# Kernel optimization log

Measured on AMD Instinct MI355X. Metric: run time of the kernel, lower is better.

Reference implementation:

```python
import jax, jax.numpy as jnp
import numpy as np

M = 5
N = 3
NUM_EPOC = 500
LR = 0.01


def setup_inputs() -> dict:
    key = jax.random.key(0)
    k1, k2, k3, k4, k5 = jax.random.split(key, 5)
    x = jax.random.normal(k1, (8, 32, 32, 128), dtype=jnp.float32)
    weight = jax.random.normal(k2, (3, 3, 128, 256), dtype=jnp.float32) * 0.05
    shiftPara = jax.random.normal(k3, (N,), dtype=jnp.float32) * 0.1
    beta = jax.random.normal(k4, (N,), dtype=jnp.float32)
    alphas_init = jax.random.normal(k5, (M,), dtype=jnp.float32)
    return {"x": x, "weight": weight, "shiftPara": shiftPara, "beta": beta, "alphas_init": alphas_init}


def _binary_weights(w):
    # w: (kh, kw, Cin, Cout). sign(W - mean + shift_i * std), shift_i in linspace(-1, 1, M)
    mean = jnp.mean(w)
    var = jnp.var(w)
    shifts = (-1.0 + jnp.arange(M, dtype=jnp.float32) * (2.0 / (M - 1))) * jnp.sqrt(var)  # (M,)
    return jnp.sign((w - mean)[None] + shifts.reshape(M, 1, 1, 1, 1))  # (M, kh, kw, Cin, Cout)


def _alphas(w, bw, alphas_init):
    # 500-step OLS gradient descent, faithful to the original loop
    flat_w = w.reshape(-1)            # (K,)
    flat_b = bw.reshape(M, -1)        # (M, K)
    K = flat_w.shape[0]

    def step(a, _):
        resid = flat_b.T @ a - flat_w            # (K,)
        grad = (flat_b @ resid) / K              # (M,)
        return a - LR * grad, None

    a, _ = jax.lax.scan(step, alphas_init, None, length=NUM_EPOC)
    return a


def reference(x, weight, shiftPara, beta, alphas_init):
    B, H, W, Cin = x.shape
    kh, kw, _, Cout = weight.shape

    bw = _binary_weights(weight)                       # (M, kh, kw, Cin, Cout)
    alphas = _alphas(weight, bw, alphas_init)          # (M,)

    # N binarized input branches: sign(clip(x + shift_n, 0, 1) - 0.5)
    shifted = jnp.clip(x[None] + shiftPara.reshape(N, 1, 1, 1, 1), 0.0, 1.0)
    bx = jnp.sign(shifted - 0.5)                       # (N, B, H, W, Cin)

    # Fold the M binary bases into output channels -> single conv over N*B images
    w_all = jnp.transpose(bw, (1, 2, 3, 0, 4)).reshape(kh, kw, Cin, M * Cout)
    y = jax.lax.conv_general_dilated(
        bx.reshape(N * B, H, W, Cin), w_all,
        window_strides=(1, 1), padding="SAME",
        dimension_numbers=("NHWC", "HWIO", "NHWC"))     # (N*B, H, W, M*Cout)
    y = y.reshape(N, B, H, W, M, Cout)

    # sum_m alpha_m * conv, then sum_n beta_n * branch
    return jnp.einsum("nbhwmc,m,n->bhwc", y, alphas, beta)
```

## Files before the change

kernel.cpp:

```cpp
#include <hip/hip_runtime.h>
#include <math.h>

#define KW_ELEMS 294912
#define KW_F4    73728
#define LR_GD 0.01
#define NBLK_RED 64
#define NBLK_GC  256

typedef __attribute__((ext_vector_type(8))) short short8;
typedef __attribute__((ext_vector_type(4))) float f32x4;

#define WS_SP_OFF    0
#define WS_GP_OFF    1024
#define WS_WP_OFF    17408
#define WS_XE_OFF    607232
#define XE_CHUNKS    (8 * 34 * 34 * 16)

__device__ __forceinline__ unsigned short f2bf(float f) {
    union { float f; unsigned int u; } v; v.f = f;
    unsigned int r = v.u + 0x7fffu + ((v.u >> 16) & 1u);
    return (unsigned short)(r >> 16);
}

__device__ __forceinline__ void read_stats(const double* sp, double& sw, double& sw2) {
    int lane = threadIdx.x & 63;
    double a = sp[2 * lane];
    double b = sp[2 * lane + 1];
    #pragma unroll
    for (int off = 32; off > 0; off >>= 1) {
        a += __shfl_xor(a, off, 64);
        b += __shfl_xor(b, off, 64);
    }
    sw = a; sw2 = b;
}

__device__ __forceinline__ float xeff_one(float xv, float s0, float s1, float s2,
                                          float be0, float be1, float be2) {
    float v0 = xv + s0, v1 = xv + s1, v2 = xv + s2;
    float g0 = (v0 > 0.5f) ? 1.0f : ((v0 < 0.5f) ? -1.0f : 0.0f);
    float g1 = (v1 > 0.5f) ? 1.0f : ((v1 < 0.5f) ? -1.0f : 0.0f);
    float g2 = (v2 > 0.5f) ? 1.0f : ((v2 < 0.5f) ? -1.0f : 0.0f);
    return be0 * g0 + be1 * g1 + be2 * g2;
}

__global__ __launch_bounds__(256) void k_pre(const float* __restrict__ w,
                                             const float* __restrict__ x,
                                             const float* __restrict__ shiftp,
                                             const float* __restrict__ beta,
                                             void* __restrict__ wsv) {
    int tid = threadIdx.x;

    if (blockIdx.x < NBLK_RED) {
        double* sp = (double*)((char*)wsv + WS_SP_OFF);
        __shared__ double s1[256];
        __shared__ double s2[256];

        double a = 0.0, b = 0.0;
        for (int i = blockIdx.x * 256 + tid; i < KW_ELEMS; i += NBLK_RED * 256) {
            double v = (double)w[i];
            a += v; b += v * v;
        }
        s1[tid] = a; s2[tid] = b;
        __syncthreads();
        for (int off = 128; off > 0; off >>= 1) {
            if (tid < off) { s1[tid] += s1[tid + off]; s2[tid] += s2[tid + off]; }
            __syncthreads();
        }
        if (tid == 0) { sp[blockIdx.x * 2] = s1[0]; sp[blockIdx.x * 2 + 1] = s2[0]; }
    } else {
        unsigned short* xe = (unsigned short*)((char*)wsv + WS_XE_OFF);
        float s0 = shiftp[0], s1v = shiftp[1], s2v = shiftp[2];
        float be0 = beta[0], be1 = beta[1], be2 = beta[2];

        for (int idx = (blockIdx.x - NBLK_RED) * 256 + tid; idx < XE_CHUNKS;
             idx += 128 * 256) {
            int cb  = idx & 15;
            int c2  = idx >> 4;
            int pos = c2 % 34;
            int t   = c2 / 34;
            int row = t % 34;
            int b   = t / 34;
            int g   = row - 1;
            int wp  = pos - 1;
            unsigned short v[8] = {0, 0, 0, 0, 0, 0, 0, 0};
            if (g >= 0 && g < 32 && wp >= 0 && wp < 32) {
                const float* xp = &x[(((b * 32 + g) * 32) + wp) * 128 + cb * 8];
                float4 x0 = *(const float4*)(xp);
                float4 x1 = *(const float4*)(xp + 4);
                float e[8] = {x0.x, x0.y, x0.z, x0.w, x1.x, x1.y, x1.z, x1.w};
                #pragma unroll
                for (int j = 0; j < 8; j++)
                    v[j] = f2bf(xeff_one(e[j], s0, s1v, s2v, be0, be1, be2));
            }
            int dst = c2 * 256 + ((cb * 16) ^ ((pos & 7) << 4));
            *(short8*)((char*)xe + dst) = *(short8*)v;
        }
    }
}

__global__ __launch_bounds__(256) void k_gc(const float* __restrict__ w,
                                            void* __restrict__ wsv) {
    const double* sp = (const double*)((const char*)wsv + WS_SP_OFF);
    char* gp = (char*)wsv + WS_GP_OFF;

    __shared__ int    lg[4][5];
    __shared__ double lc[4][5];

    int tid  = threadIdx.x;
    int lane = tid & 63;
    int wave = tid >> 6;

    double sw, sw2;
    read_stats(sp, sw, sw2);
    double mean = sw / (double)KW_ELEMS;
    double var  = sw2 / (double)KW_ELEMS - mean * mean;
    float meanf = (float)mean;
    float sigf  = sqrtf((float)var);

    float thr[5];
    #pragma unroll
    for (int m = 0; m < 5; m++) thr[m] = (1.0f - 0.5f * (float)m) * sigf;

    int   cnt[5] = {0, 0, 0, 0, 0};
    float ss[5]  = {0.f, 0.f, 0.f, 0.f, 0.f};
    for (int i4 = blockIdx.x * 256 + tid; i4 < KW_F4; i4 += NBLK_GC * 256) {
        float4 v = *(const float4*)(&w[i4 * 4]);
        float e[4] = {v.x, v.y, v.z, v.w};
        #pragma unroll
        for (int j = 0; j < 4; j++) {
            float base = e[j] - meanf;
            #pragma unroll
            for (int m = 0; m < 5; m++) {
                bool bel = base < thr[m];
                cnt[m] += bel ? 1 : 0;
                ss[m]  += bel ? e[j] : 0.f;
            }
        }
    }
    double sd[5];
    #pragma unroll
    for (int m = 0; m < 5; m++) sd[m] = (double)ss[m];
    #pragma unroll
    for (int m = 0; m < 5; m++) {
        int c = cnt[m]; double s = sd[m];
        #pragma unroll
        for (int off = 32; off > 0; off >>= 1) {
            c += __shfl_xor(c, off, 64);
            s += __shfl_xor(s, off, 64);
        }
        cnt[m] = c; sd[m] = s;
    }
    if (lane == 0) {
        #pragma unroll
        for (int m = 0; m < 5; m++) { lg[wave][m] = cnt[m]; lc[wave][m] = sd[m]; }
    }
    __syncthreads();
    if (tid == 0) {
        int*    pn = (int*)(gp + blockIdx.x * 64);
        double* pS = (double*)(gp + blockIdx.x * 64 + 24);
        #pragma unroll
        for (int m = 0; m < 5; m++) {
            pn[m] = lg[0][m] + lg[1][m] + lg[2][m] + lg[3][m];
            pS[m] = lc[0][m] + lc[1][m] + lc[2][m] + lc[3][m];
        }
    }
}

__global__ __launch_bounds__(256) void k_weff(const float* __restrict__ w,
                                              const float* __restrict__ a0f,
                                              void* __restrict__ wsv) {
    const double* sp = (const double*)((const char*)wsv + WS_SP_OFF);
    const char*   gp = (const char*)wsv + WS_GP_OFF;
    unsigned short* wpk = (unsigned short*)((char*)wsv + WS_WP_OFF);

    __shared__ double Gd[25], Am[25], Rm[25], Tm[25];
    __shared__ double astar_s[5];
    __shared__ float  alph[5];
    __shared__ float  tile[32][64];

    int tid   = threadIdx.x;
    int lane  = tid & 63;
    int tap   = blockIdx.x >> 4;
    int rest  = blockIdx.x & 15;
    int c32   = rest >> 2;
    int cin0  = c32 * 32;
    int cout0 = (rest & 3) * 64;

    int i0 = tid, i1 = tid + 256;
    int ci0 = i0 >> 4, f40 = i0 & 15;
    int ci1 = i1 >> 4, f41 = i1 & 15;
    float4 v0 = *(const float4*)(&w[(tap * 128 + cin0 + ci0) * 256 + cout0 + f40 * 4]);
    float4 v1 = *(const float4*)(&w[(tap * 128 + cin0 + ci1) * 256 + cout0 + f41 * 4]);

    double sw, sw2;
    read_stats(sp, sw, sw2);
    double mean = sw / (double)KW_ELEMS;
    double var  = sw2 / (double)KW_ELEMS - mean * mean;
    float meanf = (float)mean;
    float sigf  = sqrtf((float)var);

    int nred[5]; double Sred[5];
    #pragma unroll
    for (int m = 0; m < 5; m++) { nred[m] = 0; Sred[m] = 0.0; }
    #pragma unroll
    for (int q = 0; q < 4; q++) {
        const int*    pn = (const int*)(gp + (lane + q * 64) * 64);
        const double* pS = (const double*)(gp + (lane + q * 64) * 64 + 24);
        #pragma unroll
        for (int m = 0; m < 5; m++) { nred[m] += pn[m]; Sred[m] += pS[m]; }
    }
    #pragma unroll
    for (int m = 0; m < 5; m++) {
        int c = nred[m]; double s = Sred[m];
        #pragma unroll
        for (int off = 32; off > 0; off >>= 1) {
            c += __shfl_xor(c, off, 64);
            s += __shfl_xor(s, off, 64);
        }
        nred[m] = c; Sred[m] = s;
    }
    double Creg[5];
    #pragma unroll
    for (int m = 0; m < 5; m++)
        Creg[m] = (sw - 2.0 * Sred[m]) / (double)KW_ELEMS;

    if (tid < 25) {
        int i = tid / 5, j = tid % 5;
        double v;
        if (i == j) v = 1.0;
        else {
            int d = nred[i] - nred[j];
            if (d < 0) d = -d;
            v = ((double)KW_ELEMS - 2.0 * (double)d) / (double)KW_ELEMS;
        }
        Gd[tid] = v;
        double a = ((i == j) ? 1.0 : 0.0) - LR_GD * v;
        Am[tid] = a;
        Rm[tid] = a;
    }
    __syncthreads();

    if (tid == 64) {
        double L[25];
        #pragma unroll
        for (int i = 0; i < 25; i++) L[i] = 0.0;
        #pragma unroll
        for (int i = 0; i < 5; i++) {
            #pragma unroll
            for (int j = 0; j <= i; j++) {
                double s = Gd[i * 5 + j];
                #pragma unroll
                for (int k = 0; k < j; k++) s -= L[i * 5 + k] * L[j * 5 + k];
                if (i == j) L[i * 5 + j] = sqrt(s);
                else        L[i * 5 + j] = s / L[j * 5 + j];
            }
        }
        double y[5], astar[5];
        #pragma unroll
        for (int i = 0; i < 5; i++) {
            double s = Creg[i];
            #pragma unroll
            for (int k = 0; k < i; k++) s -= L[i * 5 + k] * y[k];
            y[i] = s / L[i * 5 + i];
        }
        #pragma unroll
        for (int ii2 = 0; ii2 < 5; ii2++) {
            int i = 4 - ii2;
            double s = y[i];
            #pragma unroll
            for (int k = 0; k < 5; k++) if (k > i) s -= L[k * 5 + i] * astar[k];
            astar[i] = s / L[i * 5 + i];
        }
        #pragma unroll
        for (int i = 0; i < 5; i++) astar_s[i] = astar[i];
    }

    {
        int i = tid / 5, j = tid % 5;
        const int bits[8] = {1, 1, 1, 1, 0, 1, 0, 0};
        #pragma unroll
        for (int s = 0; s < 8; s++) {
            double tv = 0.0;
            if (tid < 25) {
                #pragma unroll
                for (int k = 0; k < 5; k++) tv += Rm[i * 5 + k] * Rm[k * 5 + j];
                Tm[tid] = tv;
            }
            __syncthreads();
            double rv = tv;
            if (tid < 25) {
                if (bits[s]) {
                    rv = 0.0;
                    #pragma unroll
                    for (int k = 0; k < 5; k++) rv += Tm[i * 5 + k] * Am[k * 5 + j];
                }
                Rm[tid] = rv;
            }
            __syncthreads();
        }
    }

    if (tid < 5) {
        double s = astar_s[tid];
        #pragma unroll
        for (int j = 0; j < 5; j++)
            s += Rm[tid * 5 + j] * ((double)a0f[j] - astar_s[j]);
        alph[tid] = (float)s;
    }
    __syncthreads();

    float al[5] = {alph[0], alph[1], alph[2], alph[3], alph[4]};

    {
        float r[4] = {v0.x, v0.y, v0.z, v0.w};
        #pragma unroll
        for (int j = 0; j < 4; j++) {
            float base = r[j] - meanf;
            float acc = 0.0f;
            #pragma unroll
            for (int m = 0; m < 5; m++) {
                float arg = base + (-1.0f + 0.5f * (float)m) * sigf;
                float s = (arg > 0.0f) ? 1.0f : ((arg < 0.0f) ? -1.0f : 0.0f);
                acc += al[m] * s;
            }
            tile[ci0][f40 * 4 + j] = acc;
        }
        float r1[4] = {v1.x, v1.y, v1.z, v1.w};
        #pragma unroll
        for (int j = 0; j < 4; j++) {
            float base = r1[j] - meanf;
            float acc = 0.0f;
            #pragma unroll
            for (int m = 0; m < 5; m++) {
                float arg = base + (-1.0f + 0.5f * (float)m) * sigf;
                float s = (arg > 0.0f) ? 1.0f : ((arg < 0.0f) ? -1.0f : 0.0f);
                acc += al[m] * s;
            }
            tile[ci1][f41 * 4 + j] = acc;
        }
    }
    __syncthreads();

    int cc  = tid & 63;
    int kg  = tid >> 6;
    unsigned short ob[8];
    #pragma unroll
    for (int k = 0; k < 8; k++) ob[k] = f2bf(tile[kg * 8 + k][cc]);
    unsigned short* dst = wpk + (((tap * 16 + c32 * 4 + kg) * 256) + cout0 + cc) * 8;
    *(short8*)dst = *(short8*)ob;
}

__global__ __launch_bounds__(256, 2) void k_conv(
    const void* __restrict__ wsv, float* __restrict__ out) {
    const unsigned short* wp = (const unsigned short*)((const char*)wsv + WS_WP_OFF);
    const char* xe = (const char*)wsv + WS_XE_OFF;
    __shared__ __align__(16) unsigned short ldsx[3 * 34 * 128];

    int bid = blockIdx.x;
    int ch  = bid & 1;
    int h   = (bid >> 1) & 31;
    int b   = bid >> 6;
    int tid = threadIdx.x;

    const char* src = xe + ((b * 34 + h) * 34) * 256;
    #pragma unroll 2
    for (int i = tid; i < 1632; i += 256) {
        *(short8*)((char*)ldsx + i * 16) = *(const short8*)(src + i * 16);
    }
    __syncthreads();

    int lane = tid & 63;
    int wave = tid >> 6;
    int l15  = lane & 15;
    int kg   = lane >> 4;
    int coutbase = (ch << 7) + wave * 32;

    f32x4 acc[2][2];
    #pragma unroll
    for (int mt = 0; mt < 2; mt++)
        #pragma unroll
        for (int nt = 0; nt < 2; nt++) acc[mt][nt] = (f32x4){0.f, 0.f, 0.f, 0.f};

    const unsigned short* wbase = wp + ((kg * 256) + coutbase + l15) * 8;

    short8 bc[8], bn[8];
    #pragma unroll
    for (int q = 0; q < 4; q++) {
        bc[2 * q]     = *(const short8*)(wbase + q * 8192);
        bc[2 * q + 1] = *(const short8*)(wbase + q * 8192 + 128);
    }

    #pragma unroll
    for (int dh = 0; dh < 3; dh++) {
        #pragma unroll
        for (int dw = 0; dw < 3; dw++) {
            int tap = dh * 3 + dw;
            if (tap < 8) {
                const unsigned short* wnx = wbase + (tap + 1) * 32768;
                #pragma unroll
                for (int q = 0; q < 4; q++) {
                    bn[2 * q]     = *(const short8*)(wnx + q * 8192);
                    bn[2 * q + 1] = *(const short8*)(wnx + q * 8192 + 128);
                }
            }
            int r0  = dh * 34 + l15 + dw;
            int r1  = r0 + 16;
            int key = ((l15 + dw) & 7) << 4;
            #pragma unroll
            for (int q = 0; q < 4; q++) {
                int cbyte = q * 64 + kg * 16;
                short8 a0f8 = *(const short8*)((const char*)ldsx +
                               (r0 * 256 + (cbyte ^ key)));
                short8 a1f8 = *(const short8*)((const char*)ldsx +
                               (r1 * 256 + (cbyte ^ key)));
                acc[0][0] = __builtin_amdgcn_mfma_f32_16x16x32_bf16(a0f8, bc[2*q],   acc[0][0], 0, 0, 0);
                acc[0][1] = __builtin_amdgcn_mfma_f32_16x16x32_bf16(a0f8, bc[2*q+1], acc[0][1], 0, 0, 0);
                acc[1][0] = __builtin_amdgcn_mfma_f32_16x16x32_bf16(a1f8, bc[2*q],   acc[1][0], 0, 0, 0);
                acc[1][1] = __builtin_amdgcn_mfma_f32_16x16x32_bf16(a1f8, bc[2*q+1], acc[1][1], 0, 0, 0);
            }
            if (tap < 8) {
                #pragma unroll
                for (int i = 0; i < 8; i++) bc[i] = bn[i];
            }
        }
    }

    #pragma unroll
    for (int mt = 0; mt < 2; mt++) {
        #pragma unroll
        for (int nt = 0; nt < 2; nt++) {
            int col = coutbase + nt * 16 + l15;
            #pragma unroll
            for (int reg = 0; reg < 4; reg++) {
                int row = mt * 16 + kg * 4 + reg;
                out[(((b * 32 + h) * 32) + row) * 256 + col] = acc[mt][nt][reg];
            }
        }
    }
}

extern "C" void kernel_launch(void* const* d_in, const int* in_sizes, int n_in,
                              void* d_out, int out_size, void* d_ws, size_t ws_size,
                              hipStream_t stream) {
    const float* x      = (const float*)d_in[0];
    const float* w      = (const float*)d_in[1];
    const float* shiftp = (const float*)d_in[2];
    const float* beta   = (const float*)d_in[3];
    const float* a0     = (const float*)d_in[4];
    float* out = (float*)d_out;

    k_pre<<<192, 256, 0, stream>>>(w, x, shiftp, beta, d_ws);
    k_gc<<<NBLK_GC, 256, 0, stream>>>(w, d_ws);
    k_weff<<<144, 256, 0, stream>>>(w, a0, d_ws);
    k_conv<<<512, 256, 0, stream>>>(d_ws, out);
}
```

Baseline: 33.46 us.

## Use wave shuffles for matrix power, vectorize stats reduction, widen x-encode grid

The 25-thread matrix exponentiation by squaring in k_weff now keeps each matrix element in a register and exchanges values with wavefront shuffles instead of shared memory, which removes the 16 block-wide barriers. The weight mean/variance reduction in k_pre now loads float4 instead of scalars. The x-encoding part of k_pre gets 192 blocks instead of 128. Together these aim to cut barrier latency in the small serial section and raise memory throughput in the preprocessing kernel, at the cost of launching more blocks.

```diff
diff --git a/kernel.cpp b/kernel.cpp
--- a/kernel.cpp
+++ b/kernel.cpp
@@ -5,6 +5,7 @@
 #define KW_F4    73728
 #define LR_GD 0.01
 #define NBLK_RED 64
+#define NBLK_XE  192
 #define NBLK_GC  256
 
 typedef __attribute__((ext_vector_type(8))) short short8;
@@ -56,9 +57,11 @@
         __shared__ double s2[256];
 
         double a = 0.0, b = 0.0;
-        for (int i = blockIdx.x * 256 + tid; i < KW_ELEMS; i += NBLK_RED * 256) {
-            double v = (double)w[i];
-            a += v; b += v * v;
+        for (int i4 = blockIdx.x * 256 + tid; i4 < KW_F4; i4 += NBLK_RED * 256) {
+            float4 v = *(const float4*)(&w[i4 * 4]);
+            a += (double)v.x + (double)v.y + (double)v.z + (double)v.w;
+            b += (double)v.x * (double)v.x + (double)v.y * (double)v.y
+               + (double)v.z * (double)v.z + (double)v.w * (double)v.w;
         }
         s1[tid] = a; s2[tid] = b;
         __syncthreads();
@@ -73,7 +76,7 @@
         float be0 = beta[0], be1 = beta[1], be2 = beta[2];
 
         for (int idx = (blockIdx.x - NBLK_RED) * 256 + tid; idx < XE_CHUNKS;
-             idx += 128 * 256) {
+             idx += NBLK_XE * 256) {
             int cb  = idx & 15;
             int c2  = idx >> 4;
             int pos = c2 % 34;
@@ -173,7 +176,8 @@
     const char*   gp = (const char*)wsv + WS_GP_OFF;
     unsigned short* wpk = (unsigned short*)((char*)wsv + WS_WP_OFF);
 
-    __shared__ double Gd[25], Am[25], Rm[25], Tm[25];
+    __shared__ double Gd[25];
+    __shared__ double RmL[25];
     __shared__ double astar_s[5];
     __shared__ float  alph[5];
     __shared__ float  tile[32][64];
@@ -224,19 +228,21 @@
     for (int m = 0; m < 5; m++)
         Creg[m] = (sw - 2.0 * Sred[m]) / (double)KW_ELEMS;
 
-    if (tid < 25) {
+    double Rg = 0.0, Ag = 0.0;
+    {
         int i = tid / 5, j = tid % 5;
-        double v;
-        if (i == j) v = 1.0;
-        else {
-            int d = nred[i] - nred[j];
-            if (d < 0) d = -d;
-            v = ((double)KW_ELEMS - 2.0 * (double)d) / (double)KW_ELEMS;
-        }
-        Gd[tid] = v;
-        double a = ((i == j) ? 1.0 : 0.0) - LR_GD * v;
-        Am[tid] = a;
-        Rm[tid] = a;
+        if (tid < 25) {
+            double v;
+            if (i == j) v = 1.0;
+            else {
+                int d = nred[i] - nred[j];
+                if (d < 0) d = -d;
+                v = ((double)KW_ELEMS - 2.0 * (double)d) / (double)KW_ELEMS;
+            }
+            Gd[tid] = v;
+            Ag = ((i == j) ? 1.0 : 0.0) - LR_GD * v;
+            Rg = Ag;
+        }
     }
     __syncthreads();
 
@@ -275,36 +281,40 @@
         for (int i = 0; i < 5; i++) astar_s[i] = astar[i];
     }
 
-    {
+    if (tid < 25) {
         int i = tid / 5, j = tid % 5;
         const int bits[8] = {1, 1, 1, 1, 0, 1, 0, 0};
         #pragma unroll
         for (int s = 0; s < 8; s++) {
-            double tv = 0.0;
-            if (tid < 25) {
+            double t = 0.0;
+            #pragma unroll
+            for (int k = 0; k < 5; k++) {
+                double rik = __shfl(Rg, i * 5 + k, 64);
+                double rkj = __shfl(Rg, k * 5 + j, 64);
+                t += rik * rkj;
+            }
+            if (bits[s]) {
+                double r2 = 0.0;
                 #pragma unroll
-                for (int k = 0; k < 5; k++) tv += Rm[i * 5 + k] * Rm[k * 5 + j];
-                Tm[tid] = tv;
-            }
-            __syncthreads();
-            double rv = tv;
-            if (tid < 25) {
-                if (bits[s]) {
-                    rv = 0.0;
-                    #pragma unroll
-                    for (int k = 0; k < 5; k++) rv += Tm[i * 5 + k] * Am[k * 5 + j];
+                for (int k = 0; k < 5; k++) {
+                    double tik = __shfl(t, i * 5 + k, 64);
+                    double akj = __shfl(Ag, k * 5 + j, 64);
+                    r2 += tik * akj;
                 }
-                Rm[tid] = rv;
-            }
-            __syncthreads();
-        }
-    }
+                Rg = r2;
+            } else {
+                Rg = t;
+            }
+        }
+        RmL[tid] = Rg;
+    }
+    __syncthreads();
 
     if (tid < 5) {
         double s = astar_s[tid];
         #pragma unroll
         for (int j = 0; j < 5; j++)
-            s += Rm[tid * 5 + j] * ((double)a0f[j] - astar_s[j]);
+            s += RmL[tid * 5 + j] * ((double)a0f[j] - astar_s[j]);
         alph[tid] = (float)s;
     }
     __syncthreads();
@@ -449,7 +459,7 @@
     const float* a0     = (const float*)d_in[4];
     float* out = (float*)d_out;
 
-    k_pre<<<192, 256, 0, stream>>>(w, x, shiftp, beta, d_ws);
+    k_pre<<<NBLK_RED + NBLK_XE, 256, 0, stream>>>(w, x, shiftp, beta, d_ws);
     k_gc<<<NBLK_GC, 256, 0, stream>>>(w, d_ws);
     k_weff<<<144, 256, 0, stream>>>(w, a0, d_ws);
     k_conv<<<512, 256, 0, stream>>>(d_ws, out);
```

After: 30.49 us, median of 2. -8.9%, faster.
